# Performance work log

Measured on AMD Instinct MI355X. Metric: run time of the kernel, lower is better.

The kernel has to match this reference:

```python
import jax, jax.numpy as jnp
import numpy as np

D_MODEL = 1024
NHEAD = 16
DH = D_MODEL // NHEAD  # 64
B, S = 4, 2048
SCALE = float(np.sqrt(D_MODEL))  # note: sqrt(d_model), not sqrt(dh)


def setup_inputs() -> dict:
    key = jax.random.key(0)
    ks = jax.random.split(key, 8)
    inputs = jax.random.normal(ks[0], (B, S, D_MODEL), dtype=jnp.float32)
    mask = jax.random.normal(ks[1], (B, S, S), dtype=jnp.float32) * 0.1
    # Linear weights stored as [in, out] so y = x @ W + b (equivalent to torch x @ W.T + b)
    std = 1.0 / np.sqrt(D_MODEL)
    Wq = jax.random.normal(ks[2], (D_MODEL, DH), dtype=jnp.float32) * std
    Wk = jax.random.normal(ks[3], (D_MODEL, DH), dtype=jnp.float32) * std
    Wv = jax.random.normal(ks[4], (D_MODEL, DH), dtype=jnp.float32) * std
    bq = jnp.zeros((DH,), dtype=jnp.float32)
    bk = jnp.zeros((DH,), dtype=jnp.float32)
    bv = jnp.zeros((DH,), dtype=jnp.float32)
    return {"inputs": inputs, "mask": mask, "Wq": Wq, "bq": bq,
            "Wk": Wk, "bk": bk, "Wv": Wv, "bv": bv}


def reference(inputs, mask, Wq, bq, Wk, bk, Wv, bv):
    # Projections: [B,S,d_model] -> [B,S,dh]
    Q = inputs @ Wq + bq
    K = inputs @ Wk + bk
    V = inputs @ Wv + bv
    # scores: [B, S_q, S_k]
    scores = jnp.einsum("bqd,bkd->bqk", Q, K) / SCALE
    # Faithful quirk: softmax over dim=1 (the QUERY axis), not the key axis
    probs = jax.nn.softmax(scores, axis=1)
    # Faithful quirk: mask added AFTER softmax
    A = jnp.einsum("bqk,bkd->bqd", probs + mask, V)
    return A
```

## Files before the change

### kernel.cpp

```cpp
#include <hip/hip_runtime.h>

#define NB 4
#define SS 2048
#define DMODEL 1024
#define DHEAD 64

typedef __bf16 bf16x8 __attribute__((ext_vector_type(8)));
typedef __bf16 bf16x4 __attribute__((ext_vector_type(4)));
typedef float f32x4 __attribute__((ext_vector_type(4)));

#define MFMA16(a, b, c) __builtin_amdgcn_mfma_f32_16x16x32_bf16((a), (b), (c), 0, 0, 0)


__global__ __launch_bounds__(256) void k0_wt3(
    const float* __restrict__ Wq, const float* __restrict__ Wk,
    const float* __restrict__ Wv, __bf16* __restrict__ Wt3)
{
    int idx = blockIdx.x * 256 + threadIdx.x;
    int kc = idx / 768;
    int rem = idx - kc * 768;
    int f = rem >> 6;
    int lane = rem & 63;
    int g = lane >> 4, l15 = lane & 15;
    int mode = f >> 2, nt = f & 3;
    const float* W = (mode == 0) ? Wq : (mode == 1 ? Wk : Wv);
    const float s = (mode == 0) ? 0.03125f : 1.0f;
    int n = nt * 16 + l15;
    int k = kc * 32 + g * 8;
    bf16x8 o;
    #pragma unroll
    for (int i = 0; i < 8; ++i)
        o[i] = (__bf16)(W[(size_t)(k + i) * DHEAD + n] * s);
    *(bf16x8*)(Wt3 + (size_t)idx * 8) = o;
}

#define XST 1032
__global__ __launch_bounds__(256) void k1_fused(
    const float* __restrict__ x, const __bf16* __restrict__ Wt3,
    const float* __restrict__ bq, const float* __restrict__ bk,
    const float* __restrict__ bv,
    __bf16* __restrict__ Qo, __bf16* __restrict__ Kb3, __bf16* __restrict__ Vt3)
{
    __shared__ char smem[43008];
    __bf16* stage = (__bf16*)smem;
    __bf16* outQ = (__bf16*)(smem + 36864);
    __bf16* outK = outQ + 1024;
    __bf16* outV = outK + 1024;
    const int tid = threadIdx.x;
    const int wid = tid >> 6;
    const int lane = tid & 63;
    const int l15 = lane & 15;
    const int g = lane >> 4;
    const int row0 = blockIdx.x * 16;
    const int b  = row0 >> 11;
    const int s0 = row0 & 2047;
    const int soff = (s0 >> 3) & 2;

    {
        const float* xsrc = x + (size_t)row0 * DMODEL;
        #pragma unroll
        for (int it = 0; it < 16; ++it) {
            int idx = it * 256 + tid;
            int row = idx >> 8;
            int col = (idx & 255) * 4;
            f32x4 v = *(const f32x4*)(xsrc + (size_t)row * DMODEL + col);
            bf16x4 b4;
            #pragma unroll
            for (int i = 0; i < 4; ++i) b4[i] = (__bf16)v[i];
            *(bf16x4*)(stage + row * XST + col) = b4;
        }
    }
    __syncthreads();

    f32x4 acc[12];
    #pragma unroll
    for (int f = 0; f < 12; ++f) acc[f] = (f32x4){0.f, 0.f, 0.f, 0.f};

    #pragma unroll
    for (int c = 0; c < 8; ++c) {
        bf16x8 af = *(const bf16x8*)(stage + l15 * XST + wid * 256 + c * 32 + g * 8);
        const int kc = wid * 8 + c;
        #pragma unroll
        for (int f = 0; f < 12; ++f) {
            bf16x8 bfr = *(const bf16x8*)(Wt3 + (((size_t)kc * 12 + f) << 9) + lane * 8);
            acc[f] = MFMA16(af, bfr, acc[f]);
        }
    }
    __syncthreads();
    f32x4* red = (f32x4*)smem;
    if (wid != 0) {
        #pragma unroll
        for (int f = 0; f < 12; ++f) red[((wid - 1) * 12 + f) * 64 + lane] = acc[f];
    }
    __syncthreads();
    if (wid == 0) {
        #pragma unroll
        for (int f = 0; f < 12; ++f) {
            f32x4 a = acc[f] + red[(0 * 12 + f) * 64 + lane]
                    + red[(1 * 12 + f) * 64 + lane] + red[(2 * 12 + f) * 64 + lane];
            const int md = f >> 2, nt = f & 3;
            const int n = nt * 16 + l15;
            const float* bias = (md == 0) ? bq : (md == 1 ? bk : bv);
            const float bscale = (md == 0) ? 0.03125f : 1.0f;
            float bvl = bias[n] * bscale;
            #pragma unroll
            for (int r = 0; r < 4; ++r) {
                float o = a[r] + bvl;
                int g4r = g * 4 + r;
                if (md == 0) {
                    outQ[g4r * 64 + n] = (__bf16)o;
                } else if (md == 1) {
                    int ln = ((nt & 1) * 2 + (l15 >> 3)) * 16 + g4r;
                    outK[(nt >> 1) * 512 + ln * 8 + (l15 & 7)] = (__bf16)o;
                } else {
                    outV[nt * 256 + ((g4r >> 3) * 16 + l15) * 8 + (g4r & 7)] = (__bf16)o;
                }
            }
        }
    }
    __syncthreads();
    if (tid < 128) {
        *(bf16x8*)(Qo + ((size_t)b * SS + s0) * DHEAD + tid * 8) = *(bf16x8*)(outQ + tid * 8);
        int nt = tid >> 5, e = (tid & 31) * 8;
        *(bf16x8*)(Vt3 + (((size_t)(b * 256 + (s0 >> 5) * 4 + nt)) << 9) + soff * 128 + e)
            = *(bf16x8*)(outV + nt * 256 + e);
    } else {
        int t2 = tid - 128;
        *(bf16x8*)(Kb3 + (((size_t)b * 256 + (s0 >> 4) * 2) << 9) + t2 * 8) = *(bf16x8*)(outK + t2 * 8);
    }
}

#define QST 72
__global__ __launch_bounds__(256) void k2_cs(
    const __bf16* __restrict__ Qb, const __bf16* __restrict__ Kb3,
    float* __restrict__ partial)
{
    __shared__ __bf16 qt[128 * QST];
    const int tid = threadIdx.x;
    const int wid = tid >> 6;
    const int lane = tid & 63;
    const int l15 = lane & 15;
    const int g = lane >> 4;
    const int bx = blockIdx.x;
    const int b  = bx >> 8;
    const int rem = bx & 255;
    const int kg = rem >> 4;
    const int qs = rem & 15;
    const int k0 = kg * 128 + wid * 32;

    {
        const __bf16* qsrc = Qb + ((size_t)(b * SS + qs * 128)) * DHEAD;
        #pragma unroll
        for (int it = 0; it < 4; ++it) {
            int idx = it * 256 + tid;
            int row = idx >> 3;
            int col = (idx & 7) * 8;
            *(bf16x8*)(qt + row * QST + col) = *(const bf16x8*)(qsrc + (size_t)idx * 8);
        }
    }

    const __bf16* kfr = Kb3 + (((size_t)b * 256 + (k0 >> 4) * 2) << 9) + lane * 8;
    bf16x8 ka00 = *(const bf16x8*)(kfr);
    bf16x8 ka01 = *(const bf16x8*)(kfr + 512);
    bf16x8 ka10 = *(const bf16x8*)(kfr + 1024);
    bf16x8 ka11 = *(const bf16x8*)(kfr + 1536);
    __syncthreads();

    f32x4 cs0 = (f32x4){0.f, 0.f, 0.f, 0.f};
    f32x4 cs1 = (f32x4){0.f, 0.f, 0.f, 0.f};

    #pragma unroll 2
    for (int j = 0; j < 8; ++j) {
        const __bf16* qr = qt + (j * 16 + l15) * QST + g * 8;
        bf16x8 qb0 = *(const bf16x8*)(qr);
        bf16x8 qb1 = *(const bf16x8*)(qr + 32);
        f32x4 s0 = (f32x4){0.f, 0.f, 0.f, 0.f};
        s0 = MFMA16(ka00, qb0, s0);
        s0 = MFMA16(ka01, qb1, s0);
        f32x4 s1 = (f32x4){0.f, 0.f, 0.f, 0.f};
        s1 = MFMA16(ka10, qb0, s1);
        s1 = MFMA16(ka11, qb1, s1);
        #pragma unroll
        for (int r = 0; r < 4; ++r) {
            cs0[r] += __expf(s0[r]);
            cs1[r] += __expf(s1[r]);
        }
    }
    #pragma unroll
    for (int off = 1; off < 16; off <<= 1) {
        #pragma unroll
        for (int r = 0; r < 4; ++r) {
            cs0[r] += __shfl_xor(cs0[r], off);
            cs1[r] += __shfl_xor(cs1[r], off);
        }
    }
    if (l15 == 0) {
        float* pp = partial + (size_t)qs * (NB * SS) + b * SS + k0 + 4 * g;
        *(f32x4*)(pp)      = cs0;
        *(f32x4*)(pp + 16) = cs1;
    }
}

__global__ __launch_bounds__(512) void kab(
    const __bf16* __restrict__ Qb, const __bf16* __restrict__ Kb3,
    const __bf16* __restrict__ Vt3, const float* __restrict__ mask,
    const float* __restrict__ part, float* __restrict__ out)
{
    __shared__ char smem[40960];
    float* rl = (float*)smem;
    f32x4* red = (f32x4*)(smem + 8192);
    const int tid = threadIdx.x;
    const int wid = tid >> 6;
    const int lane = tid & 63;
    const int l15 = lane & 15;
    const int g = lane >> 4;
    const int b  = blockIdx.x >> 7;
    const int q0 = (blockIdx.x & 127) * 16;

    {
        const int k = tid * 4;
        f32x4 s = (f32x4){0.f, 0.f, 0.f, 0.f};
        #pragma unroll
        for (int qs = 0; qs < 16; ++qs)
            s += *(const f32x4*)(part + (size_t)qs * (NB * SS) + b * SS + k);
        f32x4 rr;
        #pragma unroll
        for (int r = 0; r < 4; ++r) rr[r] = 1.0f / s[r];
        *(f32x4*)(rl + k) = rr;
    }

    const __bf16* qp = Qb + ((size_t)(b * SS + q0 + l15)) * DHEAD + g * 8;
    bf16x8 qb0 = *(const bf16x8*)(qp);
    bf16x8 qb1 = *(const bf16x8*)(qp + 32);
    __syncthreads();

    f32x4 acc[4];
    #pragma unroll
    for (int nt = 0; nt < 4; ++nt) acc[nt] = (f32x4){0.f, 0.f, 0.f, 0.f};
    const float* mrow = mask + ((size_t)(b * SS + q0 + (lane >> 2))) * SS + (lane & 3) * 8;
    const int msrc = l15 * 4 + g;

    #pragma unroll 2
    for (int st = 0; st < 8; ++st) {
        const int kbase = wid * 256 + st * 32;
        const __bf16* kfr = Kb3 + (((size_t)b * 256 + (kbase >> 4) * 2) << 9) + lane * 8;
        bf16x8 ka00 = *(const bf16x8*)(kfr);
        bf16x8 ka01 = *(const bf16x8*)(kfr + 512);
        bf16x8 ka10 = *(const bf16x8*)(kfr + 1024);
        bf16x8 ka11 = *(const bf16x8*)(kfr + 1536);
        const __bf16* vfr = Vt3 + (((size_t)b * 256 + (kbase >> 5) * 4) << 9) + lane * 8;
        bf16x8 vb0 = *(const bf16x8*)(vfr);
        bf16x8 vb1 = *(const bf16x8*)(vfr + 512);
        bf16x8 vb2 = *(const bf16x8*)(vfr + 1024);
        bf16x8 vb3 = *(const bf16x8*)(vfr + 1536);
        f32x4 mk0 = *(const f32x4*)(mrow + kbase);
        f32x4 mk1 = *(const f32x4*)(mrow + kbase + 4);

        f32x4 s0 = (f32x4){0.f, 0.f, 0.f, 0.f};
        s0 = MFMA16(ka00, qb0, s0);
        s0 = MFMA16(ka01, qb1, s0);
        f32x4 s1 = (f32x4){0.f, 0.f, 0.f, 0.f};
        s1 = MFMA16(ka10, qb0, s1);
        s1 = MFMA16(ka11, qb1, s1);

        f32x4 rv0 = *(const f32x4*)(rl + kbase + 4 * g);
        f32x4 rv1 = *(const f32x4*)(rl + kbase + 16 + 4 * g);
        f32x4 e0, e1;
        #pragma unroll
        for (int r = 0; r < 4; ++r) {
            e0[r] = __expf(s0[r]) * rv0[r];
            e1[r] = __expf(s1[r]) * rv1[r];
        }
        bf16x8 af;
        #pragma unroll
        for (int i = 0; i < 8; ++i) {
            int src = l15 + 16 * ((2 * g + (i >> 2)) & 3);
            float v0 = __shfl(e0[i & 3], src);
            float v1 = __shfl(e1[i & 3], src);
            float mval = __shfl((i < 4 ? mk0[i & 3] : mk1[i & 3]), msrc);
            af[i] = (__bf16)((g < 2 ? v0 : v1) + mval);
        }
        acc[0] = MFMA16(af, vb0, acc[0]);
        acc[1] = MFMA16(af, vb1, acc[1]);
        acc[2] = MFMA16(af, vb2, acc[2]);
        acc[3] = MFMA16(af, vb3, acc[3]);
    }
    __syncthreads();
    #pragma unroll
    for (int nt = 0; nt < 4; ++nt) red[(wid * 4 + nt) * 64 + lane] = acc[nt];
    __syncthreads();
    float* outO = (float*)smem;
    if (wid < 4) {
        const int nt = wid;
        f32x4 a = red[nt * 64 + lane];
        #pragma unroll
        for (int w = 1; w < 8; ++w) a += red[(w * 4 + nt) * 64 + lane];
        #pragma unroll
        for (int r = 0; r < 4; ++r)
            outO[(g * 4 + r) * 64 + nt * 16 + l15] = a[r];
    }
    __syncthreads();
    if (tid < 256) {
        int row = tid >> 4, col = (tid & 15) * 4;
        *(f32x4*)(out + ((size_t)(b * SS + q0 + row)) * DHEAD + col)
            = *(const f32x4*)(outO + row * 64 + col);
    }
}

extern "C" void kernel_launch(void* const* d_in, const int* in_sizes, int n_in,
                              void* d_out, int out_size, void* d_ws, size_t ws_size,
                              hipStream_t stream)
{
    const float* x    = (const float*)d_in[0];
    const float* mask = (const float*)d_in[1];
    const float* Wq   = (const float*)d_in[2];
    const float* bq   = (const float*)d_in[3];
    const float* Wk   = (const float*)d_in[4];
    const float* bk   = (const float*)d_in[5];
    const float* Wv   = (const float*)d_in[6];
    const float* bv   = (const float*)d_in[7];
    float* out = (float*)d_out;

    char* ws = (char*)d_ws;
    __bf16* Qbf  = (__bf16*)(ws);
    __bf16* Kb3  = (__bf16*)(ws + (1u << 20));
    __bf16* Vt3  = (__bf16*)(ws + (2u << 20));
    float*  part = (float*)(ws + (3u << 20));
    __bf16* Wt3  = (__bf16*)(ws + (3u << 20) + (512u << 10));

    k0_wt3<<<96, 256, 0, stream>>>(Wq, Wk, Wv, Wt3);
    k1_fused<<<512, 256, 0, stream>>>(x, Wt3, bq, bk, bv, Qbf, Kb3, Vt3);
    k2_cs<<<1024, 256, 0, stream>>>(Qbf, Kb3, part);
    kab<<<512, 512, 0, stream>>>(Qbf, Kb3, Vt3, mask, part, out);
}
```

Measured before the change: 54.92 us.

## Materialize exp scores in bf16 during column-sum pass and reuse in PV kernel

The column-sum kernel now writes the exponentiated QK^T scores as bf16 MFMA fragments to a 32MB workspace buffer, and a new PV kernel reads them instead of recomputing QK^T and exp. This removes the second QK^T matmul and the exp work from the final kernel. In exchange it adds 32MB of global writes and reads plus shuffles to reorder fragments. The old recompute path is kept as a fallback when the workspace is too small.

Result: slower. 63.35 us (+15.3%).

```diff
diff --git a/kernel.cpp b/kernel.cpp
--- a/kernel.cpp
+++ b/kernel.cpp
@@ -131,9 +131,10 @@
 }
 
 #define QST 72
+template<bool STOREP>
 __global__ __launch_bounds__(256) void k2_cs(
     const __bf16* __restrict__ Qb, const __bf16* __restrict__ Kb3,
-    float* __restrict__ partial)
+    float* __restrict__ partial, __bf16* __restrict__ Pf)
 {
     __shared__ __bf16 qt[128 * QST];
     const int tid = threadIdx.x;
@@ -180,10 +181,22 @@
         f32x4 s1 = (f32x4){0.f, 0.f, 0.f, 0.f};
         s1 = MFMA16(ka10, qb0, s1);
         s1 = MFMA16(ka11, qb1, s1);
-        #pragma unroll
-        for (int r = 0; r < 4; ++r) {
-            cs0[r] += __expf(s0[r]);
-            cs1[r] += __expf(s1[r]);
+        f32x4 e0, e1;
+        #pragma unroll
+        for (int r = 0; r < 4; ++r) { e0[r] = __expf(s0[r]); e1[r] = __expf(s1[r]); }
+        cs0 += e0;
+        cs1 += e1;
+        if (STOREP) {
+            bf16x8 af;
+            #pragma unroll
+            for (int i = 0; i < 8; ++i) {
+                int src = l15 + 16 * ((2 * g + (i >> 2)) & 3);
+                float v0 = __shfl(e0[i & 3], src);
+                float v1 = __shfl(e1[i & 3], src);
+                af[i] = (__bf16)(g < 2 ? v0 : v1);
+            }
+            size_t fid = ((size_t)(b * 128 + qs * 8 + j)) * 64 + (kg * 4 + wid);
+            *(bf16x8*)(Pf + (fid << 9) + lane * 8) = af;
         }
     }
     #pragma unroll
@@ -201,10 +214,10 @@
     }
 }
 
-__global__ __launch_bounds__(512) void kab(
-    const __bf16* __restrict__ Qb, const __bf16* __restrict__ Kb3,
-    const __bf16* __restrict__ Vt3, const float* __restrict__ mask,
-    const float* __restrict__ part, float* __restrict__ out)
+__global__ __launch_bounds__(512) void kab_pv(
+    const __bf16* __restrict__ Pf, const __bf16* __restrict__ Vt3,
+    const float* __restrict__ mask, const float* __restrict__ part,
+    float* __restrict__ out)
 {
     __shared__ char smem[40960];
     float* rl = (float*)smem;
@@ -216,6 +229,7 @@
     const int g = lane >> 4;
     const int b  = blockIdx.x >> 7;
     const int q0 = (blockIdx.x & 127) * 16;
+    const int qt = q0 >> 4;
 
     {
         const int k = tid * 4;
@@ -228,7 +242,91 @@
         for (int r = 0; r < 4; ++r) rr[r] = 1.0f / s[r];
         *(f32x4*)(rl + k) = rr;
     }
-
+    __syncthreads();
+
+    f32x4 acc[4];
+    #pragma unroll
+    for (int nt = 0; nt < 4; ++nt) acc[nt] = (f32x4){0.f, 0.f, 0.f, 0.f};
+    const float* mrow = mask + ((size_t)(b * SS + q0 + (lane >> 2))) * SS + (lane & 3) * 8;
+    const int msrc = l15 * 4 + g;
+    const __bf16* pfb = Pf + (((size_t)(b * 128 + qt)) * 64 << 9) + lane * 8;
+
+    #pragma unroll 2
+    for (int st = 0; st < 8; ++st) {
+        const int kbase = wid * 256 + st * 32;
+        const int kc = kbase >> 5;
+        bf16x8 pf = *(const bf16x8*)(pfb + ((size_t)kc << 9));
+        const __bf16* vfr = Vt3 + (((size_t)b * 256 + kc * 4) << 9) + lane * 8;
+        bf16x8 vb0 = *(const bf16x8*)(vfr);
+        bf16x8 vb1 = *(const bf16x8*)(vfr + 512);
+        bf16x8 vb2 = *(const bf16x8*)(vfr + 1024);
+        bf16x8 vb3 = *(const bf16x8*)(vfr + 1536);
+        f32x4 mk0 = *(const f32x4*)(mrow + kbase);
+        f32x4 mk1 = *(const f32x4*)(mrow + kbase + 4);
+        f32x4 rvA = *(const f32x4*)(rl + kbase + g * 8);
+        f32x4 rvB = *(const f32x4*)(rl + kbase + g * 8 + 4);
+
+        bf16x8 af;
+        #pragma unroll
+        for (int i = 0; i < 8; ++i) {
+            float mval = __shfl((i < 4 ? mk0[i & 3] : mk1[i & 3]), msrc);
+            float rv = (i < 4) ? rvA[i & 3] : rvB[i & 3];
+            af[i] = (__bf16)((float)pf[i] * rv + mval);
+        }
+        acc[0] = MFMA16(af, vb0, acc[0]);
+        acc[1] = MFMA16(af, vb1, acc[1]);
+        acc[2] = MFMA16(af, vb2, acc[2]);
+        acc[3] = MFMA16(af, vb3, acc[3]);
+    }
+    __syncthreads();
+    #pragma unroll
+    for (int nt = 0; nt < 4; ++nt) red[(wid * 4 + nt) * 64 + lane] = acc[nt];
+    __syncthreads();
+    float* outO = (float*)smem;
+    if (wid < 4) {
+        const int nt = wid;
+        f32x4 a = red[nt * 64 + lane];
+        #pragma unroll
+        for (int w = 1; w < 8; ++w) a += red[(w * 4 + nt) * 64 + lane];
+        #pragma unroll
+        for (int r = 0; r < 4; ++r)
+            outO[(g * 4 + r) * 64 + nt * 16 + l15] = a[r];
+    }
+    __syncthreads();
+    if (tid < 256) {
+        int row = tid >> 4, col = (tid & 15) * 4;
+        *(f32x4*)(out + ((size_t)(b * SS + q0 + row)) * DHEAD + col)
+            = *(const f32x4*)(outO + row * 64 + col);
+    }
+}
+
+__global__ __launch_bounds__(512) void kab_fb(
+    const __bf16* __restrict__ Qb, const __bf16* __restrict__ Kb3,
+    const __bf16* __restrict__ Vt3, const float* __restrict__ mask,
+    const float* __restrict__ part, float* __restrict__ out)
+{
+    __shared__ char smem[40960];
+    float* rl = (float*)smem;
+    f32x4* red = (f32x4*)(smem + 8192);
+    const int tid = threadIdx.x;
+    const int wid = tid >> 6;
+    const int lane = tid & 63;
+    const int l15 = lane & 15;
+    const int g = lane >> 4;
+    const int b  = blockIdx.x >> 7;
+    const int q0 = (blockIdx.x & 127) * 16;
+
+    {
+        const int k = tid * 4;
+        f32x4 s = (f32x4){0.f, 0.f, 0.f, 0.f};
+        #pragma unroll
+        for (int qs = 0; qs < 16; ++qs)
+            s += *(const f32x4*)(part + (size_t)qs * (NB * SS) + b * SS + k);
+        f32x4 rr;
+        #pragma unroll
+        for (int r = 0; r < 4; ++r) rr[r] = 1.0f / s[r];
+        *(f32x4*)(rl + k) = rr;
+    }
     const __bf16* qp = Qb + ((size_t)(b * SS + q0 + l15)) * DHEAD + g * 8;
     bf16x8 qb0 = *(const bf16x8*)(qp);
     bf16x8 qb1 = *(const bf16x8*)(qp + 32);
@@ -327,9 +425,16 @@
     __bf16* Vt3  = (__bf16*)(ws + (2u << 20));
     float*  part = (float*)(ws + (3u << 20));
     __bf16* Wt3  = (__bf16*)(ws + (3u << 20) + (512u << 10));
+    __bf16* Pf   = (__bf16*)(ws + (4u << 20));
+    const bool usePf = ws_size >= (36u << 20);
 
     k0_wt3<<<96, 256, 0, stream>>>(Wq, Wk, Wv, Wt3);
     k1_fused<<<512, 256, 0, stream>>>(x, Wt3, bq, bk, bv, Qbf, Kb3, Vt3);
-    k2_cs<<<1024, 256, 0, stream>>>(Qbf, Kb3, part);
-    kab<<<512, 512, 0, stream>>>(Qbf, Kb3, Vt3, mask, part, out);
-}
+    if (usePf) {
+        k2_cs<true><<<1024, 256, 0, stream>>>(Qbf, Kb3, part, Pf);
+        kab_pv<<<512, 512, 0, stream>>>(Pf, Vt3, mask, part, out);
+    } else {
+        k2_cs<false><<<1024, 256, 0, stream>>>(Qbf, Kb3, part, Pf);
+        kab_fb<<<512, 512, 0, stream>>>(Qbf, Kb3, Vt3, mask, part, out);
+    }
+}
```

## Fuse projection, column-sum and attention kernels into one persistent kernel with grid barriers

Applied to the files above, without the earlier changes.

Three launches (projection, column-sum partials, attention output) are merged into a single 512-block, 256-thread kernel that separates the phases with atomic-counter grid barriers, each block handling two column-sum tiles. The goal is to remove per-launch overhead and tail gaps between kernels. Other changes come along: an XOR-swizzled LDS layout replaces padding in the projection, the reduction is split into two rounds so shared memory shrinks to 32 KB, and the attention phase moves to 4 waves with 16 steps each, reading mask values directly instead of through shuffles. The risks are that all 512 blocks must be co-resident or the barrier will deadlock until its timeout, and that halving the waves per attention block cuts parallelism there.

Measured after the change: 217.2 us. +295.4%, slower.

```diff
diff --git a/kernel.cpp b/kernel.cpp
--- a/kernel.cpp
+++ b/kernel.cpp
@@ -12,10 +12,27 @@
 #define MFMA16(a, b, c) __builtin_amdgcn_mfma_f32_16x16x32_bf16((a), (b), (c), 0, 0, 0)
 
 
-__global__ __launch_bounds__(256) void k0_wt3(
+__device__ __forceinline__ void grid_barrier(int* cnt, int nb)
+{
+    __threadfence();
+    __syncthreads();
+    if (threadIdx.x == 0) {
+        atomicAdd(cnt, 1);
+        long long t0 = clock64();
+        while (atomicAdd(cnt, 0) < nb) {
+            __builtin_amdgcn_s_sleep(8);
+            if (clock64() - t0 > 200000000LL) break;
+        }
+    }
+    __syncthreads();
+    __threadfence();
+}
+
+__global__ __launch_bounds__(256) void k0init(
     const float* __restrict__ Wq, const float* __restrict__ Wk,
-    const float* __restrict__ Wv, __bf16* __restrict__ Wt3)
-{
+    const float* __restrict__ Wv, __bf16* __restrict__ Wt3, int* __restrict__ bar)
+{
+    if (blockIdx.x == 0 && threadIdx.x < 8) bar[threadIdx.x] = 0;
     int idx = blockIdx.x * 256 + threadIdx.x;
     int kc = idx / 768;
     int rem = idx - kc * 768;
@@ -34,24 +51,19 @@
     *(bf16x8*)(Wt3 + (size_t)idx * 8) = o;
 }
 
-#define XST 1032
-__global__ __launch_bounds__(256) void k1_fused(
-    const float* __restrict__ x, const __bf16* __restrict__ Wt3,
+__device__ __forceinline__ void phase_k1(
+    char* smem, const float* __restrict__ x, const __bf16* __restrict__ Wt3,
     const float* __restrict__ bq, const float* __restrict__ bk,
     const float* __restrict__ bv,
-    __bf16* __restrict__ Qo, __bf16* __restrict__ Kb3, __bf16* __restrict__ Vt3)
-{
-    __shared__ char smem[43008];
-    __bf16* stage = (__bf16*)smem;
-    __bf16* outQ = (__bf16*)(smem + 36864);
-    __bf16* outK = outQ + 1024;
-    __bf16* outV = outK + 1024;
+    __bf16* __restrict__ Qo, __bf16* __restrict__ Kb3, __bf16* __restrict__ Vt3,
+    int bx)
+{
     const int tid = threadIdx.x;
     const int wid = tid >> 6;
     const int lane = tid & 63;
     const int l15 = lane & 15;
     const int g = lane >> 4;
-    const int row0 = blockIdx.x * 16;
+    const int row0 = bx * 16;
     const int b  = row0 >> 11;
     const int s0 = row0 & 2047;
     const int soff = (s0 >> 3) & 2;
@@ -60,14 +72,13 @@
         const float* xsrc = x + (size_t)row0 * DMODEL;
         #pragma unroll
         for (int it = 0; it < 16; ++it) {
-            int idx = it * 256 + tid;
-            int row = idx >> 8;
-            int col = (idx & 255) * 4;
-            f32x4 v = *(const f32x4*)(xsrc + (size_t)row * DMODEL + col);
+            int row = it;
+            int byte = tid * 8;
+            f32x4 v = *(const f32x4*)(xsrc + (size_t)row * DMODEL + tid * 4);
             bf16x4 b4;
             #pragma unroll
             for (int i = 0; i < 4; ++i) b4[i] = (__bf16)v[i];
-            *(bf16x4*)(stage + row * XST + col) = b4;
+            *(bf16x4*)(smem + row * 2048 + (byte ^ ((row & 7) << 4))) = b4;
         }
     }
     __syncthreads();
@@ -76,9 +87,11 @@
     #pragma unroll
     for (int f = 0; f < 12; ++f) acc[f] = (f32x4){0.f, 0.f, 0.f, 0.f};
 
+    const int swzrow = (l15 & 7) << 4;
     #pragma unroll
     for (int c = 0; c < 8; ++c) {
-        bf16x8 af = *(const bf16x8*)(stage + l15 * XST + wid * 256 + c * 32 + g * 8);
+        int byte = (wid * 256 + c * 32 + g * 8) * 2;
+        bf16x8 af = *(const bf16x8*)(smem + l15 * 2048 + (byte ^ swzrow));
         const int kc = wid * 8 + c;
         #pragma unroll
         for (int f = 0; f < 12; ++f) {
@@ -86,34 +99,42 @@
             acc[f] = MFMA16(af, bfr, acc[f]);
         }
     }
-    __syncthreads();
+
     f32x4* red = (f32x4*)smem;
-    if (wid != 0) {
-        #pragma unroll
-        for (int f = 0; f < 12; ++f) red[((wid - 1) * 12 + f) * 64 + lane] = acc[f];
-    }
-    __syncthreads();
-    if (wid == 0) {
-        #pragma unroll
-        for (int f = 0; f < 12; ++f) {
-            f32x4 a = acc[f] + red[(0 * 12 + f) * 64 + lane]
-                    + red[(1 * 12 + f) * 64 + lane] + red[(2 * 12 + f) * 64 + lane];
-            const int md = f >> 2, nt = f & 3;
-            const int n = nt * 16 + l15;
-            const float* bias = (md == 0) ? bq : (md == 1 ? bk : bv);
-            const float bscale = (md == 0) ? 0.03125f : 1.0f;
-            float bvl = bias[n] * bscale;
+    __bf16* outQ = (__bf16*)(smem + 18432);
+    __bf16* outK = outQ + 1024;
+    __bf16* outV = outK + 1024;
+    for (int rd = 0; rd < 2; ++rd) {
+        __syncthreads();
+        if (wid != 0) {
             #pragma unroll
-            for (int r = 0; r < 4; ++r) {
-                float o = a[r] + bvl;
-                int g4r = g * 4 + r;
-                if (md == 0) {
-                    outQ[g4r * 64 + n] = (__bf16)o;
-                } else if (md == 1) {
-                    int ln = ((nt & 1) * 2 + (l15 >> 3)) * 16 + g4r;
-                    outK[(nt >> 1) * 512 + ln * 8 + (l15 & 7)] = (__bf16)o;
-                } else {
-                    outV[nt * 256 + ((g4r >> 3) * 16 + l15) * 8 + (g4r & 7)] = (__bf16)o;
+            for (int f6 = 0; f6 < 6; ++f6)
+                red[((wid - 1) * 6 + f6) * 64 + lane] = acc[rd * 6 + f6];
+        }
+        __syncthreads();
+        if (wid == 0) {
+            #pragma unroll
+            for (int f6 = 0; f6 < 6; ++f6) {
+                const int f = rd * 6 + f6;
+                f32x4 a = acc[f] + red[(0 * 6 + f6) * 64 + lane]
+                        + red[(1 * 6 + f6) * 64 + lane] + red[(2 * 6 + f6) * 64 + lane];
+                const int md = f >> 2, nt = f & 3;
+                const int n = nt * 16 + l15;
+                const float* bias = (md == 0) ? bq : (md == 1 ? bk : bv);
+                const float bscale = (md == 0) ? 0.03125f : 1.0f;
+                float bvl = bias[n] * bscale;
+                #pragma unroll
+                for (int r = 0; r < 4; ++r) {
+                    float o = a[r] + bvl;
+                    int g4r = g * 4 + r;
+                    if (md == 0) {
+                        outQ[g4r * 64 + n] = (__bf16)o;
+                    } else if (md == 1) {
+                        int ln = ((nt & 1) * 2 + (l15 >> 3)) * 16 + g4r;
+                        outK[(nt >> 1) * 512 + ln * 8 + (l15 & 7)] = (__bf16)o;
+                    } else {
+                        outV[nt * 256 + ((g4r >> 3) * 16 + l15) * 8 + (g4r & 7)] = (__bf16)o;
+                    }
                 }
             }
         }
@@ -131,23 +152,23 @@
 }
 
 #define QST 72
-__global__ __launch_bounds__(256) void k2_cs(
-    const __bf16* __restrict__ Qb, const __bf16* __restrict__ Kb3,
-    float* __restrict__ partial)
-{
-    __shared__ __bf16 qt[128 * QST];
+__device__ __forceinline__ void phase_k2(
+    char* smem, const __bf16* __restrict__ Qb, const __bf16* __restrict__ Kb3,
+    float* __restrict__ partial, int bx)
+{
+    __bf16* qt = (__bf16*)smem;
     const int tid = threadIdx.x;
     const int wid = tid >> 6;
     const int lane = tid & 63;
     const int l15 = lane & 15;
     const int g = lane >> 4;
-    const int bx = blockIdx.x;
     const int b  = bx >> 8;
     const int rem = bx & 255;
     const int kg = rem >> 4;
     const int qs = rem & 15;
     const int k0 = kg * 128 + wid * 32;
 
+    __syncthreads();
     {
         const __bf16* qsrc = Qb + ((size_t)(b * SS + qs * 128)) * DHEAD;
         #pragma unroll
@@ -201,12 +222,11 @@
     }
 }
 
-__global__ __launch_bounds__(512) void kab(
-    const __bf16* __restrict__ Qb, const __bf16* __restrict__ Kb3,
+__device__ __forceinline__ void phase_kab(
+    char* smem, const __bf16* __restrict__ Qb, const __bf16* __restrict__ Kb3,
     const __bf16* __restrict__ Vt3, const float* __restrict__ mask,
-    const float* __restrict__ part, float* __restrict__ out)
-{
-    __shared__ char smem[40960];
+    const float* __restrict__ part, float* __restrict__ out, int bx)
+{
     float* rl = (float*)smem;
     f32x4* red = (f32x4*)(smem + 8192);
     const int tid = threadIdx.x;
@@ -214,19 +234,25 @@
     const int lane = tid & 63;
     const int l15 = lane & 15;
     const int g = lane >> 4;
-    const int b  = blockIdx.x >> 7;
-    const int q0 = (blockIdx.x & 127) * 16;
-
+    const int b  = bx >> 7;
+    const int q0 = (bx & 127) * 16;
+
+    __syncthreads();
     {
-        const int k = tid * 4;
-        f32x4 s = (f32x4){0.f, 0.f, 0.f, 0.f};
-        #pragma unroll
-        for (int qs = 0; qs < 16; ++qs)
-            s += *(const f32x4*)(part + (size_t)qs * (NB * SS) + b * SS + k);
-        f32x4 rr;
-        #pragma unroll
-        for (int r = 0; r < 4; ++r) rr[r] = 1.0f / s[r];
-        *(f32x4*)(rl + k) = rr;
+        const int k = tid * 8;
+        f32x4 sa = (f32x4){0.f, 0.f, 0.f, 0.f};
+        f32x4 sb = (f32x4){0.f, 0.f, 0.f, 0.f};
+        #pragma unroll
+        for (int qs = 0; qs < 16; ++qs) {
+            const float* pp = part + (size_t)qs * (NB * SS) + b * SS + k;
+            sa += *(const f32x4*)(pp);
+            sb += *(const f32x4*)(pp + 4);
+        }
+        f32x4 ra, rb;
+        #pragma unroll
+        for (int r = 0; r < 4; ++r) { ra[r] = 1.0f / sa[r]; rb[r] = 1.0f / sb[r]; }
+        *(f32x4*)(rl + k) = ra;
+        *(f32x4*)(rl + k + 4) = rb;
     }
 
     const __bf16* qp = Qb + ((size_t)(b * SS + q0 + l15)) * DHEAD + g * 8;
@@ -237,12 +263,11 @@
     f32x4 acc[4];
     #pragma unroll
     for (int nt = 0; nt < 4; ++nt) acc[nt] = (f32x4){0.f, 0.f, 0.f, 0.f};
-    const float* mrow = mask + ((size_t)(b * SS + q0 + (lane >> 2))) * SS + (lane & 3) * 8;
-    const int msrc = l15 * 4 + g;
+    const float* mrowA = mask + ((size_t)(b * SS + q0 + l15)) * SS + g * 8;
 
     #pragma unroll 2
-    for (int st = 0; st < 8; ++st) {
-        const int kbase = wid * 256 + st * 32;
+    for (int st = 0; st < 16; ++st) {
+        const int kbase = wid * 512 + st * 32;
         const __bf16* kfr = Kb3 + (((size_t)b * 256 + (kbase >> 4) * 2) << 9) + lane * 8;
         bf16x8 ka00 = *(const bf16x8*)(kfr);
         bf16x8 ka01 = *(const bf16x8*)(kfr + 512);
@@ -253,8 +278,8 @@
         bf16x8 vb1 = *(const bf16x8*)(vfr + 512);
         bf16x8 vb2 = *(const bf16x8*)(vfr + 1024);
         bf16x8 vb3 = *(const bf16x8*)(vfr + 1536);
-        f32x4 mk0 = *(const f32x4*)(mrow + kbase);
-        f32x4 mk1 = *(const f32x4*)(mrow + kbase + 4);
+        f32x4 mk0 = *(const f32x4*)(mrowA + kbase);
+        f32x4 mk1 = *(const f32x4*)(mrowA + kbase + 4);
 
         f32x4 s0 = (f32x4){0.f, 0.f, 0.f, 0.f};
         s0 = MFMA16(ka00, qb0, s0);
@@ -277,8 +302,7 @@
             int src = l15 + 16 * ((2 * g + (i >> 2)) & 3);
             float v0 = __shfl(e0[i & 3], src);
             float v1 = __shfl(e1[i & 3], src);
-            float mval = __shfl((i < 4 ? mk0[i & 3] : mk1[i & 3]), msrc);
-            af[i] = (__bf16)((g < 2 ? v0 : v1) + mval);
+            af[i] = (__bf16)((g < 2 ? v0 : v1) + (i < 4 ? mk0[i & 3] : mk1[i & 3]));
         }
         acc[0] = MFMA16(af, vb0, acc[0]);
         acc[1] = MFMA16(af, vb1, acc[1]);
@@ -290,21 +314,41 @@
     for (int nt = 0; nt < 4; ++nt) red[(wid * 4 + nt) * 64 + lane] = acc[nt];
     __syncthreads();
     float* outO = (float*)smem;
-    if (wid < 4) {
-        const int nt = wid;
-        f32x4 a = red[nt * 64 + lane];
-        #pragma unroll
-        for (int w = 1; w < 8; ++w) a += red[(w * 4 + nt) * 64 + lane];
-        #pragma unroll
-        for (int r = 0; r < 4; ++r)
-            outO[(g * 4 + r) * 64 + nt * 16 + l15] = a[r];
-    }
-    __syncthreads();
-    if (tid < 256) {
+    if (wid == 0) {
+        #pragma unroll
+        for (int nt = 0; nt < 4; ++nt) {
+            f32x4 a = red[nt * 64 + lane] + red[(4 + nt) * 64 + lane]
+                    + red[(8 + nt) * 64 + lane] + red[(12 + nt) * 64 + lane];
+            #pragma unroll
+            for (int r = 0; r < 4; ++r)
+                outO[(g * 4 + r) * 64 + nt * 16 + l15] = a[r];
+        }
+    }
+    __syncthreads();
+    {
         int row = tid >> 4, col = (tid & 15) * 4;
         *(f32x4*)(out + ((size_t)(b * SS + q0 + row)) * DHEAD + col)
             = *(const f32x4*)(outO + row * 64 + col);
     }
+}
+
+__global__ __launch_bounds__(256) void mega(
+    const float* __restrict__ x, const float* __restrict__ mask,
+    const float* __restrict__ bq, const float* __restrict__ bk,
+    const float* __restrict__ bv,
+    __bf16* __restrict__ Qbf, __bf16* __restrict__ Kb3, __bf16* __restrict__ Vt3,
+    float* __restrict__ part, const __bf16* __restrict__ Wt3,
+    int* __restrict__ bar, float* __restrict__ out)
+{
+    __shared__ char smem[32768];
+    const int nb = gridDim.x;
+
+    phase_k1(smem, x, Wt3, bq, bk, bv, Qbf, Kb3, Vt3, blockIdx.x);
+    grid_barrier(&bar[0], nb);
+    phase_k2(smem, Qbf, Kb3, part, blockIdx.x * 2);
+    phase_k2(smem, Qbf, Kb3, part, blockIdx.x * 2 + 1);
+    grid_barrier(&bar[1], nb);
+    phase_kab(smem, Qbf, Kb3, Vt3, mask, part, out, blockIdx.x);
 }
 
 extern "C" void kernel_launch(void* const* d_in, const int* in_sizes, int n_in,
@@ -327,9 +371,8 @@
     __bf16* Vt3  = (__bf16*)(ws + (2u << 20));
     float*  part = (float*)(ws + (3u << 20));
     __bf16* Wt3  = (__bf16*)(ws + (3u << 20) + (512u << 10));
-
-    k0_wt3<<<96, 256, 0, stream>>>(Wq, Wk, Wv, Wt3);
-    k1_fused<<<512, 256, 0, stream>>>(x, Wt3, bq, bk, bv, Qbf, Kb3, Vt3);
-    k2_cs<<<1024, 256, 0, stream>>>(Qbf, Kb3, part);
-    kab<<<512, 512, 0, stream>>>(Qbf, Kb3, Vt3, mask, part, out);
-}
+    int*    bar  = (int*)(ws + (3u << 20) + (512u << 10) + (384u << 10));
+
+    k0init<<<96, 256, 0, stream>>>(Wq, Wk, Wv, Wt3, bar);
+    mega<<<512, 256, 0, stream>>>(x, mask, bq, bk, bv, Qbf, Kb3, Vt3, part, Wt3, bar, out);
+}
```

## Split mask@V into separate blocks co-launched with column-sum kernel

Applied to the files above, without the earlier changes.

Uses linearity (probs+mask)@V = probs@V + mask@V to compute the mask@V product in extra blocks of the column-sum kernel, which does not depend on the softmax normalizers. The final kernel then only computes probs@V and adds its result to the output written earlier. This moves the 64MB mask stream off the critical path of the dependent kernel so it overlaps with the compute-bound column-sum work. The cost is an extra read-modify-write of the output and a larger second launch.

After: 63.14 us. +15.0%, slower.

```diff
diff --git a/kernel.cpp b/kernel.cpp
--- a/kernel.cpp
+++ b/kernel.cpp
@@ -131,80 +131,141 @@
 }
 
 #define QST 72
-__global__ __launch_bounds__(256) void k2_cs(
+__global__ __launch_bounds__(256) void k2mv(
     const __bf16* __restrict__ Qb, const __bf16* __restrict__ Kb3,
-    float* __restrict__ partial)
-{
-    __shared__ __bf16 qt[128 * QST];
+    const __bf16* __restrict__ Vt3, const float* __restrict__ mask,
+    float* __restrict__ partial, float* __restrict__ out)
+{
+    __shared__ char smem[20480];
     const int tid = threadIdx.x;
     const int wid = tid >> 6;
     const int lane = tid & 63;
     const int l15 = lane & 15;
     const int g = lane >> 4;
-    const int bx = blockIdx.x;
-    const int b  = bx >> 8;
-    const int rem = bx & 255;
-    const int kg = rem >> 4;
-    const int qs = rem & 15;
-    const int k0 = kg * 128 + wid * 32;
-
-    {
-        const __bf16* qsrc = Qb + ((size_t)(b * SS + qs * 128)) * DHEAD;
-        #pragma unroll
-        for (int it = 0; it < 4; ++it) {
-            int idx = it * 256 + tid;
-            int row = idx >> 3;
-            int col = (idx & 7) * 8;
-            *(bf16x8*)(qt + row * QST + col) = *(const bf16x8*)(qsrc + (size_t)idx * 8);
-        }
-    }
-
-    const __bf16* kfr = Kb3 + (((size_t)b * 256 + (k0 >> 4) * 2) << 9) + lane * 8;
-    bf16x8 ka00 = *(const bf16x8*)(kfr);
-    bf16x8 ka01 = *(const bf16x8*)(kfr + 512);
-    bf16x8 ka10 = *(const bf16x8*)(kfr + 1024);
-    bf16x8 ka11 = *(const bf16x8*)(kfr + 1536);
-    __syncthreads();
-
-    f32x4 cs0 = (f32x4){0.f, 0.f, 0.f, 0.f};
-    f32x4 cs1 = (f32x4){0.f, 0.f, 0.f, 0.f};
-
-    #pragma unroll 2
-    for (int j = 0; j < 8; ++j) {
-        const __bf16* qr = qt + (j * 16 + l15) * QST + g * 8;
-        bf16x8 qb0 = *(const bf16x8*)(qr);
-        bf16x8 qb1 = *(const bf16x8*)(qr + 32);
-        f32x4 s0 = (f32x4){0.f, 0.f, 0.f, 0.f};
-        s0 = MFMA16(ka00, qb0, s0);
-        s0 = MFMA16(ka01, qb1, s0);
-        f32x4 s1 = (f32x4){0.f, 0.f, 0.f, 0.f};
-        s1 = MFMA16(ka10, qb0, s1);
-        s1 = MFMA16(ka11, qb1, s1);
-        #pragma unroll
-        for (int r = 0; r < 4; ++r) {
-            cs0[r] += __expf(s0[r]);
-            cs1[r] += __expf(s1[r]);
-        }
-    }
-    #pragma unroll
-    for (int off = 1; off < 16; off <<= 1) {
-        #pragma unroll
-        for (int r = 0; r < 4; ++r) {
-            cs0[r] += __shfl_xor(cs0[r], off);
-            cs1[r] += __shfl_xor(cs1[r], off);
-        }
-    }
-    if (l15 == 0) {
-        float* pp = partial + (size_t)qs * (NB * SS) + b * SS + k0 + 4 * g;
-        *(f32x4*)(pp)      = cs0;
-        *(f32x4*)(pp + 16) = cs1;
-    }
-}
-
-__global__ __launch_bounds__(512) void kab(
+
+    if (blockIdx.x < 1024) {
+        __bf16* qt = (__bf16*)smem;
+        const int bx = blockIdx.x;
+        const int b  = bx >> 8;
+        const int rem = bx & 255;
+        const int kg = rem >> 4;
+        const int qs = rem & 15;
+        const int k0 = kg * 128 + wid * 32;
+
+        {
+            const __bf16* qsrc = Qb + ((size_t)(b * SS + qs * 128)) * DHEAD;
+            #pragma unroll
+            for (int it = 0; it < 4; ++it) {
+                int idx = it * 256 + tid;
+                int row = idx >> 3;
+                int col = (idx & 7) * 8;
+                *(bf16x8*)(qt + row * QST + col) = *(const bf16x8*)(qsrc + (size_t)idx * 8);
+            }
+        }
+
+        const __bf16* kfr = Kb3 + (((size_t)b * 256 + (k0 >> 4) * 2) << 9) + lane * 8;
+        bf16x8 ka00 = *(const bf16x8*)(kfr);
+        bf16x8 ka01 = *(const bf16x8*)(kfr + 512);
+        bf16x8 ka10 = *(const bf16x8*)(kfr + 1024);
+        bf16x8 ka11 = *(const bf16x8*)(kfr + 1536);
+        __syncthreads();
+
+        f32x4 cs0 = (f32x4){0.f, 0.f, 0.f, 0.f};
+        f32x4 cs1 = (f32x4){0.f, 0.f, 0.f, 0.f};
+
+        #pragma unroll 2
+        for (int j = 0; j < 8; ++j) {
+            const __bf16* qr = qt + (j * 16 + l15) * QST + g * 8;
+            bf16x8 qb0 = *(const bf16x8*)(qr);
+            bf16x8 qb1 = *(const bf16x8*)(qr + 32);
+            f32x4 s0 = (f32x4){0.f, 0.f, 0.f, 0.f};
+            s0 = MFMA16(ka00, qb0, s0);
+            s0 = MFMA16(ka01, qb1, s0);
+            f32x4 s1 = (f32x4){0.f, 0.f, 0.f, 0.f};
+            s1 = MFMA16(ka10, qb0, s1);
+            s1 = MFMA16(ka11, qb1, s1);
+            #pragma unroll
+            for (int r = 0; r < 4; ++r) {
+                cs0[r] += __expf(s0[r]);
+                cs1[r] += __expf(s1[r]);
+            }
+        }
+        #pragma unroll
+        for (int off = 1; off < 16; off <<= 1) {
+            #pragma unroll
+            for (int r = 0; r < 4; ++r) {
+                cs0[r] += __shfl_xor(cs0[r], off);
+                cs1[r] += __shfl_xor(cs1[r], off);
+            }
+        }
+        if (l15 == 0) {
+            float* pp = partial + (size_t)qs * (NB * SS) + b * SS + k0 + 4 * g;
+            *(f32x4*)(pp)      = cs0;
+            *(f32x4*)(pp + 16) = cs1;
+        }
+    } else {
+        f32x4* red = (f32x4*)smem;
+        float* outO = (float*)(smem + 16384);
+        const int bx2 = blockIdx.x - 1024;
+        const int b  = bx2 >> 7;
+        const int q0 = (bx2 & 127) * 16;
+
+        f32x4 acc[4];
+        #pragma unroll
+        for (int nt = 0; nt < 4; ++nt) acc[nt] = (f32x4){0.f, 0.f, 0.f, 0.f};
+        const float* mrowA = mask + ((size_t)(b * SS + q0 + l15)) * SS + g * 8;
+
+        #pragma unroll 2
+        for (int st = 0; st < 16; ++st) {
+            const int kbase = wid * 512 + st * 32;
+            const __bf16* vfr = Vt3 + (((size_t)b * 256 + (kbase >> 5) * 4) << 9) + lane * 8;
+            bf16x8 vb0 = *(const bf16x8*)(vfr);
+            bf16x8 vb1 = *(const bf16x8*)(vfr + 512);
+            bf16x8 vb2 = *(const bf16x8*)(vfr + 1024);
+            bf16x8 vb3 = *(const bf16x8*)(vfr + 1536);
+            f32x4 mk0 = *(const f32x4*)(mrowA + kbase);
+            f32x4 mk1 = *(const f32x4*)(mrowA + kbase + 4);
+            bf16x8 af;
+            #pragma unroll
+            for (int i = 0; i < 4; ++i) {
+                af[i]     = (__bf16)mk0[i];
+                af[i + 4] = (__bf16)mk1[i];
+            }
+            acc[0] = MFMA16(af, vb0, acc[0]);
+            acc[1] = MFMA16(af, vb1, acc[1]);
+            acc[2] = MFMA16(af, vb2, acc[2]);
+            acc[3] = MFMA16(af, vb3, acc[3]);
+        }
+        __syncthreads();
+        #pragma unroll
+        for (int nt = 0; nt < 4; ++nt) red[(wid * 4 + nt) * 64 + lane] = acc[nt];
+        __syncthreads();
+        if (wid == 0) {
+            f32x4 atot[4];
+            #pragma unroll
+            for (int nt = 0; nt < 4; ++nt) {
+                atot[nt] = red[nt * 64 + lane] + red[(4 + nt) * 64 + lane]
+                         + red[(8 + nt) * 64 + lane] + red[(12 + nt) * 64 + lane];
+            }
+            #pragma unroll
+            for (int nt = 0; nt < 4; ++nt)
+                #pragma unroll
+                for (int r = 0; r < 4; ++r)
+                    outO[(g * 4 + r) * 64 + nt * 16 + l15] = atot[nt][r];
+        }
+        __syncthreads();
+        {
+            int row = tid >> 4, col = (tid & 15) * 4;
+            *(f32x4*)(out + ((size_t)(b * SS + q0 + row)) * DHEAD + col)
+                = *(const f32x4*)(outO + row * 64 + col);
+        }
+    }
+}
+
+__global__ __launch_bounds__(512) void kb(
     const __bf16* __restrict__ Qb, const __bf16* __restrict__ Kb3,
-    const __bf16* __restrict__ Vt3, const float* __restrict__ mask,
-    const float* __restrict__ part, float* __restrict__ out)
+    const __bf16* __restrict__ Vt3, const float* __restrict__ part,
+    float* __restrict__ out)
 {
     __shared__ char smem[40960];
     float* rl = (float*)smem;
@@ -237,8 +298,6 @@
     f32x4 acc[4];
     #pragma unroll
     for (int nt = 0; nt < 4; ++nt) acc[nt] = (f32x4){0.f, 0.f, 0.f, 0.f};
-    const float* mrow = mask + ((size_t)(b * SS + q0 + (lane >> 2))) * SS + (lane & 3) * 8;
-    const int msrc = l15 * 4 + g;
 
     #pragma unroll 2
     for (int st = 0; st < 8; ++st) {
@@ -253,8 +312,6 @@
         bf16x8 vb1 = *(const bf16x8*)(vfr + 512);
         bf16x8 vb2 = *(const bf16x8*)(vfr + 1024);
         bf16x8 vb3 = *(const bf16x8*)(vfr + 1536);
-        f32x4 mk0 = *(const f32x4*)(mrow + kbase);
-        f32x4 mk1 = *(const f32x4*)(mrow + kbase + 4);
 
         f32x4 s0 = (f32x4){0.f, 0.f, 0.f, 0.f};
         s0 = MFMA16(ka00, qb0, s0);
@@ -277,8 +334,7 @@
             int src = l15 + 16 * ((2 * g + (i >> 2)) & 3);
             float v0 = __shfl(e0[i & 3], src);
             float v1 = __shfl(e1[i & 3], src);
-            float mval = __shfl((i < 4 ? mk0[i & 3] : mk1[i & 3]), msrc);
-            af[i] = (__bf16)((g < 2 ? v0 : v1) + mval);
+            af[i] = (__bf16)(g < 2 ? v0 : v1);
         }
         acc[0] = MFMA16(af, vb0, acc[0]);
         acc[1] = MFMA16(af, vb1, acc[1]);
@@ -302,8 +358,10 @@
     __syncthreads();
     if (tid < 256) {
         int row = tid >> 4, col = (tid & 15) * 4;
-        *(f32x4*)(out + ((size_t)(b * SS + q0 + row)) * DHEAD + col)
-            = *(const f32x4*)(outO + row * 64 + col);
+        float* dst = out + ((size_t)(b * SS + q0 + row)) * DHEAD + col;
+        f32x4 prev = *(const f32x4*)dst;
+        f32x4 val  = *(const f32x4*)(outO + row * 64 + col);
+        *(f32x4*)dst = prev + val;
     }
 }
 
@@ -330,6 +388,6 @@
 
     k0_wt3<<<96, 256, 0, stream>>>(Wq, Wk, Wv, Wt3);
     k1_fused<<<512, 256, 0, stream>>>(x, Wt3, bq, bk, bv, Qbf, Kb3, Vt3);
-    k2_cs<<<1024, 256, 0, stream>>>(Qbf, Kb3, part);
-    kab<<<512, 512, 0, stream>>>(Qbf, Kb3, Vt3, mask, part, out);
-}
+    k2mv<<<1536, 256, 0, stream>>>(Qbf, Kb3, Vt3, mask, part, out);
+    kb<<<512, 512, 0, stream>>>(Qbf, Kb3, Vt3, part, out);
+}
```
